# Optimization experiments

Hardware: AMD Instinct MI355X
Metric: run time of the kernel (lower is better)

Reference implementation:

```python
import jax, jax.numpy as jnp
import numpy as np

D = 2048      # d_model
FF = 8192     # d_ff
S = 4096      # seq_len == max_len
EPS = 1.1920929e-07  # torch.finfo(float32).eps (nn.RMSNorm default when eps=None)
SCALE = float(np.sqrt(D))


def _rms_norm(x, w):
    # x: [S, D]
    return x * jax.lax.rsqrt(jnp.mean(x * x, axis=-1, keepdims=True) + EPS) * w


def _rope(x, cos, sin):
    # x: [S, D]; cos/sin: [S, D/2]
    x1, x2 = jnp.split(x, 2, axis=-1)
    return jnp.concatenate([x1 * cos - x2 * sin, x1 * sin + x2 * cos], axis=-1)


def setup_inputs() -> dict:
    key = jax.random.key(0)
    ks = jax.random.split(key, 9)

    def w(k, shape, scale=0.02):
        return jax.random.normal(k, shape, dtype=jnp.float32) * scale

    x = jax.random.normal(ks[0], (S, D), dtype=jnp.float32)
    # torch nn.Linear stores weight as [out, in]; forward is x @ W.T
    wq = w(ks[1], (D, D))
    wk = w(ks[2], (D, D))
    wv = w(ks[3], (D, D))
    wo = w(ks[4], (D, D))
    w_gate = w(ks[5], (FF, D))
    w_up = w(ks[6], (FF, D))
    w_down = w(ks[7], (D, FF))
    w_rn1 = jnp.ones((D,), dtype=jnp.float32)
    w_rn2 = jnp.ones((D,), dtype=jnp.float32)
    # RoPE caches (buffers)
    freqs = 1.0 / 10000.0 ** (jnp.arange(0, D, 2, dtype=jnp.float32) / D)
    t = jnp.arange(S, dtype=jnp.float32)
    angles = jnp.outer(t, freqs)  # [S, D/2]
    cos = jnp.cos(angles)
    sin = jnp.sin(angles)
    return dict(x=x, w_rn1=w_rn1, wq=wq, wk=wk, wv=wv, wo=wo,
                w_rn2=w_rn2, w_gate=w_gate, w_up=w_up, w_down=w_down,
                cos=cos, sin=sin)


def reference(x, w_rn1, wq, wk, wv, wo, w_rn2, w_gate, w_up, w_down, cos, sin):
    h = _rms_norm(x, w_rn1)                      # [S, D]
    q = _rope(h @ wq.T, cos, sin)                # [S, D]
    k = _rope(h @ wk.T, cos, sin)                # [S, D]
    v = h @ wv.T                                 # [S, D]
    attn = jax.nn.softmax(q @ k.T / SCALE, axis=-1)  # [S, S]
    x = x + (attn @ v) @ wo.T                    # residual 1
    h = _rms_norm(x, w_rn2)
    ffn = (jax.nn.silu(h @ w_gate.T) * (h @ w_up.T)) @ w_down.T  # SwiGLU
    return x + ffn
```

## Files before the change

kernel.cpp:

```cpp
#include <hip/hip_runtime.h>

#define S_LEN 4096
#define D_MODEL 2048
#define FF_DIM 8192
#define QKV_LD 6144

typedef __attribute__((ext_vector_type(8))) short s16x8;
typedef __attribute__((ext_vector_type(4))) short s16x4;
typedef __attribute__((ext_vector_type(4))) float f32x4;

__device__ __forceinline__ short f2bf(float f) {
  union { float f; unsigned u; } c; c.f = f;
  unsigned r = (c.u + 0x7fffu + ((c.u >> 16) & 1u)) >> 16;
  return (short)r;
}
__device__ __forceinline__ float bf2f(short s) {
  union { unsigned u; float f; } c; c.u = ((unsigned)(unsigned short)s) << 16;
  return c.f;
}

#define GLDS16(g, l) __builtin_amdgcn_global_load_lds( \
    (const __attribute__((address_space(1))) unsigned*)(g), \
    (__attribute__((address_space(3))) unsigned*)(l), 16, 0, 0)

template <int N> __device__ __forceinline__ void waitvm() {
  if constexpr (N == 0)      asm volatile("s_waitcnt vmcnt(0)" ::: "memory");
  else if constexpr (N == 3) asm volatile("s_waitcnt vmcnt(3)" ::: "memory");
  else if constexpr (N == 4) asm volatile("s_waitcnt vmcnt(4)" ::: "memory");
  else if constexpr (N == 6) asm volatile("s_waitcnt vmcnt(6)" ::: "memory");
  else                       asm volatile("s_waitcnt vmcnt(8)" ::: "memory");
}

__device__ __forceinline__ int swz(int byte_off) {
  return byte_off ^ (((byte_off >> 9) & 1) << 5);
}

__global__ void conv_f32_bf16(const float* __restrict__ in, short* __restrict__ out, long n) {
  long i = ((long)blockIdx.x * blockDim.x + threadIdx.x) * 8;
  if (i >= n) return;
  f32x4 a = *(const f32x4*)(in + i);
  f32x4 b = *(const f32x4*)(in + i + 4);
  s16x8 o;
  o[0] = f2bf(a[0]); o[1] = f2bf(a[1]); o[2] = f2bf(a[2]); o[3] = f2bf(a[3]);
  o[4] = f2bf(b[0]); o[5] = f2bf(b[1]); o[6] = f2bf(b[2]); o[7] = f2bf(b[3]);
  *(s16x8*)(out + i) = o;
}

__global__ void rmsnorm_kernel(const float* __restrict__ x, const float* __restrict__ w,
                               short* __restrict__ out) {
  const int row = blockIdx.x;
  const int t = threadIdx.x;
  const float* xr = x + (long)row * D_MODEL;
  f32x4 v0 = ((const f32x4*)xr)[t];
  f32x4 v1 = ((const f32x4*)xr)[256 + t];
  float ss = v0[0]*v0[0] + v0[1]*v0[1] + v0[2]*v0[2] + v0[3]*v0[3]
           + v1[0]*v1[0] + v1[1]*v1[1] + v1[2]*v1[2] + v1[3]*v1[3];
  #pragma unroll
  for (int o = 32; o > 0; o >>= 1) ss += __shfl_xor(ss, o, 64);
  __shared__ float red[4];
  if ((t & 63) == 0) red[t >> 6] = ss;
  __syncthreads();
  ss = red[0] + red[1] + red[2] + red[3];
  float scale = rsqrtf(ss * (1.0f / D_MODEL) + 1.1920929e-07f);
  f32x4 w0 = ((const f32x4*)w)[t];
  f32x4 w1 = ((const f32x4*)w)[256 + t];
  s16x4 o0, o1;
  #pragma unroll
  for (int i = 0; i < 4; i++) {
    o0[i] = f2bf(v0[i] * scale * w0[i]);
    o1[i] = f2bf(v1[i] * scale * w1[i]);
  }
  short* orow = out + (long)row * D_MODEL;
  ((s16x4*)orow)[t] = o0;
  ((s16x4*)orow)[256 + t] = o1;
}

__global__ void rope_kernel(short* __restrict__ qkv,
                            const float* __restrict__ cosb, const float* __restrict__ sinb) {
  const int s = blockIdx.x;
  short* row = qkv + (long)s * QKV_LD + (blockIdx.y ? D_MODEL : 0);
  const int j = threadIdx.x * 4;
  f32x4 c = *(const f32x4*)(cosb + (long)s * (D_MODEL / 2) + j);
  f32x4 sn = *(const f32x4*)(sinb + (long)s * (D_MODEL / 2) + j);
  s16x4 x1 = *(s16x4*)(row + j);
  s16x4 x2 = *(s16x4*)(row + (D_MODEL / 2) + j);
  s16x4 o1, o2;
  #pragma unroll
  for (int i = 0; i < 4; i++) {
    float a = bf2f(x1[i]), b = bf2f(x2[i]);
    o1[i] = f2bf(a * c[i] - b * sn[i]);
    o2[i] = f2bf(a * sn[i] + b * c[i]);
  }
  *(s16x4*)(row + j) = o1;
  *(s16x4*)(row + (D_MODEL / 2) + j) = o2;
}

__global__ void transpose_kernel(const short* __restrict__ in, short* __restrict__ out,
                                 int R, int C, int ld) {
  __shared__ short tile[32][33];
  const int bx = blockIdx.x * 32, by = blockIdx.y * 32;
  const int x = threadIdx.x, y = threadIdx.y;
  #pragma unroll
  for (int i = 0; i < 32; i += 8) tile[y + i][x] = in[(long)(by + y + i) * ld + bx + x];
  __syncthreads();
  #pragma unroll
  for (int i = 0; i < 32; i += 8) out[(long)(bx + y + i) * R + by + x] = tile[x][y + i];
}

__global__ void softmax_kernel(const float* __restrict__ sraw, short* __restrict__ pb) {
  const int row = blockIdx.x;
  const int t = threadIdx.x;
  const float* rp = sraw + (long)row * S_LEN;
  f32x4 v[4];
  #pragma unroll
  for (int i = 0; i < 4; i++) v[i] = ((const f32x4*)rp)[i * 256 + t];
  float m = -1e30f;
  #pragma unroll
  for (int i = 0; i < 4; i++)
    m = fmaxf(m, fmaxf(fmaxf(v[i][0], v[i][1]), fmaxf(v[i][2], v[i][3])));
  #pragma unroll
  for (int o = 32; o > 0; o >>= 1) m = fmaxf(m, __shfl_xor(m, o, 64));
  __shared__ float redm[4], reds[4];
  if ((t & 63) == 0) redm[t >> 6] = m;
  __syncthreads();
  m = fmaxf(fmaxf(redm[0], redm[1]), fmaxf(redm[2], redm[3]));
  float sum = 0.f;
  #pragma unroll
  for (int i = 0; i < 4; i++) {
    #pragma unroll
    for (int j = 0; j < 4; j++) { v[i][j] = __expf(v[i][j] - m); sum += v[i][j]; }
  }
  #pragma unroll
  for (int o = 32; o > 0; o >>= 1) sum += __shfl_xor(sum, o, 64);
  if ((t & 63) == 0) reds[t >> 6] = sum;
  __syncthreads();
  sum = reds[0] + reds[1] + reds[2] + reds[3];
  float inv = 1.0f / sum;
  short* prow = pb + (long)row * S_LEN;
  #pragma unroll
  for (int i = 0; i < 4; i++) {
    s16x4 o;
    #pragma unroll
    for (int j = 0; j < 4; j++) o[j] = f2bf(v[i][j] * inv);
    ((s16x4*)prow)[i * 256 + t] = o;
  }
}

template <int BN, int EPI>
__global__ __launch_bounds__(512)
void gemm_pipe(const short* __restrict__ A, const short* __restrict__ B,
               float* __restrict__ Cf, short* __restrict__ Cb,
               const short* __restrict__ gmul, const float* __restrict__ res,
               int K, int lda, int ldb, int ldc, float scale) {
  constexpr int BM = 256;
  constexpr int LPS = (BN == 256) ? 4 : 3;
  constexpr int WR = (BN == 256) ? 2 : 4;
  constexpr int WC = 8 / WR;
  constexpr int MF = BM / WR / 16;
  constexpr int NF = BN / WC / 16;
  __shared__ short lds[4][(BM + BN) * 32];

  const int t = threadIdx.x;
  const int lane = t & 63, wid = t >> 6;
  const int wr = wid / WC, wc = wid % WC;
  const int llo = lane & 15, lhi = lane >> 4;

  const int nwg = gridDim.x * gridDim.y;
  int bid = blockIdx.y * gridDim.x + blockIdx.x;
  bid = (bid & 7) * (nwg >> 3) + (bid >> 3);
  const long m0 = (long)(bid / gridDim.x) * BM;
  const long n0 = (long)(bid % gridDim.x) * BN;

  const int ca0 = t, ca1 = t + 512;
  auto src_off = [&](int c, long r0, long ld) {
    int sb = swz(c * 16);
    return (r0 + (sb >> 6)) * ld + ((sb & 63) >> 1);
  };
  const long as0 = src_off(ca0, m0, lda);
  const long as1 = src_off(ca1, m0, lda);
  const long bs0 = src_off(ca0, n0, ldb);
  const long bs1 = (BN == 256) ? src_off(ca1, n0, ldb) : 0;

  f32x4 acc[MF][NF];
  #pragma unroll
  for (int m = 0; m < MF; m++)
    #pragma unroll
    for (int n = 0; n < NF; n++) acc[m][n] = (f32x4)(0.f);

  int aoff[MF], boff[NF];
  #pragma unroll
  for (int m = 0; m < MF; m++) {
    int b = (wr * (BM / WR) + m * 16 + llo) * 64 + lhi * 16;
    aoff[m] = swz(b) >> 1;
  }
  #pragma unroll
  for (int n = 0; n < NF; n++) {
    int b = (wc * (BN / WC) + n * 16 + llo) * 64 + lhi * 16;
    boff[n] = swz(b) >> 1;
  }

  auto stage = [&](int ks) {
    short* la = (short*)lds[ks & 3];
    short* lb = la + BM * 32;
    const long kk = (long)ks * 32;
    GLDS16(A + as0 + kk, la + ca0 * 8);
    GLDS16(A + as1 + kk, la + ca1 * 8);
    GLDS16(B + bs0 + kk, lb + ca0 * 8);
    if constexpr (BN == 256) GLDS16(B + bs1 + kk, lb + ca1 * 8);
  };

  auto phase_compute = [&](int ks) {
    const short* la = (const short*)lds[ks & 3];
    const short* lb = la + BM * 32;
    s16x8 af[MF], bf[NF];
    #pragma unroll
    for (int m = 0; m < MF; m++) af[m] = *(const s16x8*)(la + aoff[m]);
    #pragma unroll
    for (int n = 0; n < NF; n++) bf[n] = *(const s16x8*)(lb + boff[n]);
    __builtin_amdgcn_s_setprio(1);
    #pragma unroll
    for (int m = 0; m < MF; m++)
      #pragma unroll
      for (int n = 0; n < NF; n++)
        acc[m][n] = __builtin_amdgcn_mfma_f32_16x16x32_bf16(af[m], bf[n], acc[m][n], 0, 0, 0);
    __builtin_amdgcn_s_setprio(0);
  };

  const int NPH = K >> 5;
  stage(0); stage(1); stage(2);
  waitvm<2 * LPS>();
  __builtin_amdgcn_s_barrier();
  for (int p = 0; p < NPH - 3; ++p) {
    stage(p + 3);
    phase_compute(p);
    waitvm<2 * LPS>();
    __builtin_amdgcn_s_barrier();
  }
  phase_compute(NPH - 3);
  waitvm<LPS>();
  __builtin_amdgcn_s_barrier();
  phase_compute(NPH - 2);
  waitvm<0>();
  __builtin_amdgcn_s_barrier();
  phase_compute(NPH - 1);

  #pragma unroll
  for (int m = 0; m < MF; m++) {
    const long row0 = m0 + wr * (BM / WR) + m * 16 + lhi * 4;
    #pragma unroll
    for (int n = 0; n < NF; n++) {
      const long col = n0 + wc * (BN / WC) + n * 16 + llo;
      #pragma unroll
      for (int r = 0; r < 4; r++) {
        float v = acc[m][n][r];
        long idx = (row0 + r) * (long)ldc + col;
        if (EPI == 0) {
          Cb[idx] = f2bf(v);
        } else if (EPI == 1) {
          Cb[idx] = f2bf(v / (1.0f + __expf(-v)));
        } else if (EPI == 2) {
          Cb[idx] = f2bf(bf2f(gmul[idx]) * v);
        } else if (EPI == 3) {
          Cf[idx] = v * scale;
        } else {
          Cf[idx] = res[idx] + v;
        }
      }
    }
  }
}

extern "C" void kernel_launch(void* const* d_in, const int* in_sizes, int n_in,
                              void* d_out, int out_size, void* d_ws, size_t ws_size,
                              hipStream_t stream) {
  const float* x      = (const float*)d_in[0];
  const float* w_rn1  = (const float*)d_in[1];
  const float* wq     = (const float*)d_in[2];
  const float* wk     = (const float*)d_in[3];
  const float* wv     = (const float*)d_in[4];
  const float* wo     = (const float*)d_in[5];
  const float* w_rn2  = (const float*)d_in[6];
  const float* w_gate = (const float*)d_in[7];
  const float* w_up   = (const float*)d_in[8];
  const float* w_down = (const float*)d_in[9];
  const float* cosb   = (const float*)d_in[10];
  const float* sinb   = (const float*)d_in[11];
  float* out = (float*)d_out;

  const long S = S_LEN, D = D_MODEL, FF = FF_DIM;
  char* ws = (char*)d_ws;
  size_t off = 0;
  auto alloc = [&](size_t bytes) { void* p = ws + off; off += (bytes + 255) & ~(size_t)255; return p; };

  short* qkv  = (short*)alloc(S * QKV_LD * 2);
  short* vT   = (short*)alloc(D * S * 2);
  short* hb   = (short*)alloc(S * D * 2);
  float* x1   = (float*)alloc(S * D * 4);
  short* wbuf = (short*)alloc(FF * D * 2);
  char*  u2   = (char*)alloc(S * S * 4);
  float* sraw = (float*)u2;
  short* gbuf = (short*)u2;
  short* pb   = (short*)alloc(S * S * 2);

  const float inv_scale = 1.0f / sqrtf((float)D_MODEL);
  const long DD = D * D, FD = FF * D;
  const int convDD = (int)(DD / 8 / 256), convFD = (int)(FD / 8 / 256);
  dim3 blk(256), blk5(512);
  dim3 gQKV(3 * D_MODEL / 256, S_LEN / 256);
  dim3 gS(S_LEN / 256, S_LEN / 256);
  dim3 gN2048(D_MODEL / 128, S_LEN / 256);
  dim3 gF(FF_DIM / 256, S_LEN / 256);

  rmsnorm_kernel<<<S_LEN, 256, 0, stream>>>(x, w_rn1, hb);
  conv_f32_bf16<<<convDD, blk, 0, stream>>>(wq, wbuf, DD);
  conv_f32_bf16<<<convDD, blk, 0, stream>>>(wk, wbuf + DD, DD);
  conv_f32_bf16<<<convDD, blk, 0, stream>>>(wv, wbuf + 2 * DD, DD);
  gemm_pipe<256, 0><<<gQKV, blk5, 0, stream>>>(hb, wbuf, nullptr, qkv, nullptr, nullptr,
                                               D_MODEL, D_MODEL, D_MODEL, QKV_LD, 1.f);
  rope_kernel<<<dim3(S_LEN, 2), blk, 0, stream>>>(qkv, cosb, sinb);
  transpose_kernel<<<dim3(D_MODEL / 32, S_LEN / 32), dim3(32, 8), 0, stream>>>(
      qkv + 2 * D_MODEL, vT, S_LEN, D_MODEL, QKV_LD);
  gemm_pipe<256, 3><<<gS, blk5, 0, stream>>>(qkv, qkv + D_MODEL, sraw, nullptr, nullptr, nullptr,
                                             D_MODEL, QKV_LD, QKV_LD, S_LEN, inv_scale);
  softmax_kernel<<<S_LEN, 256, 0, stream>>>(sraw, pb);
  gemm_pipe<128, 0><<<gN2048, blk5, 0, stream>>>(pb, vT, nullptr, qkv + 2 * D_MODEL, nullptr, nullptr,
                                                 S_LEN, S_LEN, S_LEN, QKV_LD, 1.f);
  conv_f32_bf16<<<convDD, blk, 0, stream>>>(wo, wbuf, DD);
  gemm_pipe<128, 4><<<gN2048, blk5, 0, stream>>>(qkv + 2 * D_MODEL, wbuf, x1, nullptr, nullptr, x,
                                                 D_MODEL, QKV_LD, D_MODEL, D_MODEL, 1.f);
  rmsnorm_kernel<<<S_LEN, 256, 0, stream>>>(x1, w_rn2, hb);
  conv_f32_bf16<<<convFD, blk, 0, stream>>>(w_gate, wbuf, FD);
  gemm_pipe<256, 1><<<gF, blk5, 0, stream>>>(hb, wbuf, nullptr, gbuf, nullptr, nullptr,
                                             D_MODEL, D_MODEL, D_MODEL, FF_DIM, 1.f);
  conv_f32_bf16<<<convFD, blk, 0, stream>>>(w_up, wbuf, FD);
  gemm_pipe<256, 2><<<gF, blk5, 0, stream>>>(hb, wbuf, nullptr, gbuf, gbuf, nullptr,
                                             D_MODEL, D_MODEL, D_MODEL, FF_DIM, 1.f);
  conv_f32_bf16<<<convFD, blk, 0, stream>>>(w_down, wbuf, FD);
  gemm_pipe<128, 4><<<gN2048, blk5, 0, stream>>>(gbuf, wbuf, out, nullptr, nullptr, x1,
                                                 FF_DIM, FF_DIM, FF_DIM, D_MODEL, 1.f);
}
```

Measured before the change: 889.9 us.

## Replace GEMM with 8-phase ping-pong pipelined kernels using 64-wide K tiles

Replaces the generic 4-stage K=32 GEMM with two specialised kernels (256x256 and 256x128 tiles) that use K=64 tiles, a new 8-way XOR LDS swizzle, and a fine-grained schedule. The schedule splits each tile into quadrant MFMA phases, interleaving global-to-LDS loads of parts of the next tile with LDS reads and MFMAs, separated by barriers. The aim is better overlap of memory traffic with matrix-core work and fewer LDS bank conflicts. It adds many barriers and assumes K is a multiple of 128 (n256) or 64 (n128).

```diff
diff --git a/kernel.cpp b/kernel.cpp
--- a/kernel.cpp
+++ b/kernel.cpp
@@ -23,17 +23,13 @@
     (const __attribute__((address_space(1))) unsigned*)(g), \
     (__attribute__((address_space(3))) unsigned*)(l), 16, 0, 0)
 
-template <int N> __device__ __forceinline__ void waitvm() {
-  if constexpr (N == 0)      asm volatile("s_waitcnt vmcnt(0)" ::: "memory");
-  else if constexpr (N == 3) asm volatile("s_waitcnt vmcnt(3)" ::: "memory");
-  else if constexpr (N == 4) asm volatile("s_waitcnt vmcnt(4)" ::: "memory");
-  else if constexpr (N == 6) asm volatile("s_waitcnt vmcnt(6)" ::: "memory");
-  else                       asm volatile("s_waitcnt vmcnt(8)" ::: "memory");
-}
-
-__device__ __forceinline__ int swz(int byte_off) {
-  return byte_off ^ (((byte_off >> 9) & 1) << 5);
-}
+__device__ __forceinline__ int swz(int b) {
+  return b ^ (((b >> 7) & 7) << 4);
+}
+
+#define BAR()   __builtin_amdgcn_s_barrier()
+#define LGKM0() asm volatile("s_waitcnt lgkmcnt(0)" ::: "memory")
+#define VMC(n)  asm volatile("s_waitcnt vmcnt(" #n ")" ::: "memory")
 
 __global__ void conv_f32_bf16(const float* __restrict__ in, short* __restrict__ out, long n) {
   long i = ((long)blockIdx.x * blockDim.x + threadIdx.x) * 8;
@@ -146,128 +142,239 @@
   }
 }
 
-template <int BN, int EPI>
+template <int EPI>
+__device__ __forceinline__ void epi_store(float v, long idx, float* Cf, short* Cb,
+                                          const short* gmul, const float* res, float scale) {
+  if (EPI == 0)      Cb[idx] = f2bf(v);
+  else if (EPI == 1) Cb[idx] = f2bf(v / (1.0f + __expf(-v)));
+  else if (EPI == 2) Cb[idx] = f2bf(bf2f(gmul[idx]) * v);
+  else if (EPI == 3) Cf[idx] = v * scale;
+  else               Cf[idx] = res[idx] + v;
+}
+
+template <int EPI>
 __global__ __launch_bounds__(512)
-void gemm_pipe(const short* __restrict__ A, const short* __restrict__ B,
-               float* __restrict__ Cf, short* __restrict__ Cb,
-               const short* __restrict__ gmul, const float* __restrict__ res,
-               int K, int lda, int ldb, int ldc, float scale) {
-  constexpr int BM = 256;
-  constexpr int LPS = (BN == 256) ? 4 : 3;
-  constexpr int WR = (BN == 256) ? 2 : 4;
-  constexpr int WC = 8 / WR;
-  constexpr int MF = BM / WR / 16;
-  constexpr int NF = BN / WC / 16;
-  __shared__ short lds[4][(BM + BN) * 32];
-
+void gemm8p_n256(const short* __restrict__ A, const short* __restrict__ B,
+                 float* __restrict__ Cf, short* __restrict__ Cb,
+                 const short* __restrict__ gmul, const float* __restrict__ res,
+                 int K, int lda, int ldb, int ldc, float scale) {
+  __shared__ short lds[2][32768];
   const int t = threadIdx.x;
   const int lane = t & 63, wid = t >> 6;
-  const int wr = wid / WC, wc = wid % WC;
+  const int wr = wid >> 2, wc = wid & 3;
   const int llo = lane & 15, lhi = lane >> 4;
 
   const int nwg = gridDim.x * gridDim.y;
   int bid = blockIdx.y * gridDim.x + blockIdx.x;
   bid = (bid & 7) * (nwg >> 3) + (bid >> 3);
-  const long m0 = (long)(bid / gridDim.x) * BM;
-  const long n0 = (long)(bid % gridDim.x) * BN;
-
-  const int ca0 = t, ca1 = t + 512;
-  auto src_off = [&](int c, long r0, long ld) {
-    int sb = swz(c * 16);
-    return (r0 + (sb >> 6)) * ld + ((sb & 63) >> 1);
+  const long m0 = (long)(bid / gridDim.x) * 256;
+  const long n0 = (long)(bid % gridDim.x) * 256;
+
+  const int c0 = t, c1 = t + 512;
+  const int sb0 = swz(c0 * 16), sb1 = swz(c1 * 16);
+  const short* srcA0 = A + (m0 + (sb0 >> 7)) * (long)lda + ((sb0 & 127) >> 1);
+  const short* srcA1 = A + (m0 + (sb1 >> 7)) * (long)lda + ((sb1 & 127) >> 1);
+  const short* srcB0 = B + (n0 + (sb0 >> 7)) * (long)ldb + ((sb0 & 127) >> 1);
+  const short* srcB1 = B + (n0 + (sb1 >> 7)) * (long)ldb + ((sb1 & 127) >> 1);
+  const long dA = 128L * lda, dB = 128L * ldb;
+  const int NT = K >> 6, NI = NT >> 1;
+
+  int aof[4][2], bof[2][2];
+  #pragma unroll
+  for (int mf = 0; mf < 4; mf++)
+    #pragma unroll
+    for (int ks = 0; ks < 2; ks++)
+      aof[mf][ks] = swz((wr * 128 + mf * 16 + llo) * 128 + ks * 64 + lhi * 16) >> 1;
+  #pragma unroll
+  for (int nf = 0; nf < 2; nf++)
+    #pragma unroll
+    for (int ks = 0; ks < 2; ks++)
+      bof[nf][ks] = swz(32768 + (wc * 64 + nf * 16 + llo) * 128 + ks * 64 + lhi * 16) >> 1;
+
+  f32x4 acc[8][4];
+  #pragma unroll
+  for (int m = 0; m < 8; m++)
+    #pragma unroll
+    for (int n = 0; n < 4; n++) acc[m][n] = (f32x4)(0.f);
+
+  s16x8 ar[4][2], b0r[2][2], b1r[2][2];
+
+  auto stage = [&](int tt, int p) {
+    if (tt >= NT) return;
+    short* dst = (short*)lds[tt & 1] + p * 8192;
+    const long kk = (long)tt * 64;
+    const short *s0, *s1;
+    if (p == 0)      { s0 = srcA0;      s1 = srcA1; }
+    else if (p == 1) { s0 = srcA0 + dA; s1 = srcA1 + dA; }
+    else if (p == 2) { s0 = srcB0;      s1 = srcB1; }
+    else             { s0 = srcB0 + dB; s1 = srcB1 + dB; }
+    GLDS16(s0 + kk, dst + c0 * 8);
+    GLDS16(s1 + kk, dst + c1 * 8);
   };
-  const long as0 = src_off(ca0, m0, lda);
-  const long as1 = src_off(ca1, m0, lda);
-  const long bs0 = src_off(ca0, n0, ldb);
-  const long bs1 = (BN == 256) ? src_off(ca1, n0, ldb) : 0;
-
-  f32x4 acc[MF][NF];
-  #pragma unroll
-  for (int m = 0; m < MF; m++)
-    #pragma unroll
-    for (int n = 0; n < NF; n++) acc[m][n] = (f32x4)(0.f);
-
-  int aoff[MF], boff[NF];
-  #pragma unroll
-  for (int m = 0; m < MF; m++) {
-    int b = (wr * (BM / WR) + m * 16 + llo) * 64 + lhi * 16;
-    aoff[m] = swz(b) >> 1;
-  }
-  #pragma unroll
-  for (int n = 0; n < NF; n++) {
-    int b = (wc * (BN / WC) + n * 16 + llo) * 64 + lhi * 16;
-    boff[n] = swz(b) >> 1;
-  }
-
-  auto stage = [&](int ks) {
-    short* la = (short*)lds[ks & 3];
-    short* lb = la + BM * 32;
-    const long kk = (long)ks * 32;
-    GLDS16(A + as0 + kk, la + ca0 * 8);
-    GLDS16(A + as1 + kk, la + ca1 * 8);
-    GLDS16(B + bs0 + kk, lb + ca0 * 8);
-    if constexpr (BN == 256) GLDS16(B + bs1 + kk, lb + ca1 * 8);
+
+#define LDA6(BUF, MH) { const short* lp = (const short*)lds[BUF]; \
+  _Pragma("unroll") for (int mf = 0; mf < 4; mf++) \
+  _Pragma("unroll") for (int ks = 0; ks < 2; ks++) \
+    ar[mf][ks] = *(const s16x8*)(lp + aof[mf][ks] + (MH) * 4096); }
+#define LDB6(BUF, NH, DST) { const short* lp = (const short*)lds[BUF]; \
+  _Pragma("unroll") for (int nf = 0; nf < 2; nf++) \
+  _Pragma("unroll") for (int ks = 0; ks < 2; ks++) \
+    DST[nf][ks] = *(const s16x8*)(lp + bof[nf][ks] + (NH) * 2048); }
+#define MFMAQ6(MH, NH, BR) { __builtin_amdgcn_s_setprio(1); \
+  _Pragma("unroll") for (int ks = 0; ks < 2; ks++) \
+  _Pragma("unroll") for (int mf = 0; mf < 4; mf++) \
+  _Pragma("unroll") for (int nf = 0; nf < 2; nf++) \
+    acc[(MH)*4+mf][(NH)*2+nf] = __builtin_amdgcn_mfma_f32_16x16x32_bf16( \
+        ar[mf][ks], BR[nf][ks], acc[(MH)*4+mf][(NH)*2+nf], 0, 0, 0); \
+  __builtin_amdgcn_s_setprio(0); }
+
+  stage(0, 0); stage(0, 1); stage(0, 2); stage(0, 3);
+  stage(1, 2); stage(1, 3);
+  VMC(4); BAR();
+
+  for (int it = 0; it < NI; ++it) {
+    const int tt = it * 2;
+    const bool last = (it == NI - 1);
+    LDA6(0, 0); LDB6(0, 0, b0r); stage(tt + 1, 0);
+    BAR(); LGKM0(); MFMAQ6(0, 0, b0r); BAR();
+    LDB6(0, 1, b1r); stage(tt + 1, 1);
+    BAR(); LGKM0(); MFMAQ6(0, 1, b1r); BAR();
+    LDA6(0, 1); stage(tt + 2, 2);
+    BAR(); LGKM0(); MFMAQ6(1, 1, b1r); BAR();
+    stage(tt + 2, 3);
+    if (last) { VMC(0); } else { VMC(4); }
+    BAR(); MFMAQ6(1, 0, b0r); BAR();
+    LDA6(1, 0); LDB6(1, 0, b0r); stage(tt + 2, 0);
+    BAR(); LGKM0(); MFMAQ6(0, 0, b0r); BAR();
+    LDB6(1, 1, b1r); stage(tt + 2, 1);
+    BAR(); LGKM0(); MFMAQ6(0, 1, b1r); BAR();
+    LDA6(1, 1); stage(tt + 3, 2);
+    BAR(); LGKM0(); MFMAQ6(1, 1, b1r); BAR();
+    stage(tt + 3, 3);
+    if (last) { VMC(0); } else { VMC(4); }
+    BAR(); MFMAQ6(1, 0, b0r); BAR();
+  }
+
+  #pragma unroll
+  for (int mf = 0; mf < 8; mf++) {
+    const long row0 = m0 + wr * 128 + mf * 16 + lhi * 4;
+    #pragma unroll
+    for (int j = 0; j < 4; j++) {
+      const long col = n0 + wc * 64 + (j >> 1) * 32 + (j & 1) * 16 + llo;
+      #pragma unroll
+      for (int r = 0; r < 4; r++)
+        epi_store<EPI>(acc[mf][j][r], (row0 + r) * (long)ldc + col, Cf, Cb, gmul, res, scale);
+    }
+  }
+#undef LDA6
+#undef LDB6
+#undef MFMAQ6
+}
+
+template <int EPI>
+__global__ __launch_bounds__(512)
+void gemm8p_n128(const short* __restrict__ A, const short* __restrict__ B,
+                 float* __restrict__ Cf, short* __restrict__ Cb,
+                 const short* __restrict__ gmul, const float* __restrict__ res,
+                 int K, int lda, int ldb, int ldc, float scale) {
+  __shared__ short lds[3][24576];
+  const int t = threadIdx.x;
+  const int lane = t & 63, wid = t >> 6;
+  const int wr = wid >> 1, wc = wid & 1;
+  const int llo = lane & 15, lhi = lane >> 4;
+
+  const int nwg = gridDim.x * gridDim.y;
+  int bid = blockIdx.y * gridDim.x + blockIdx.x;
+  bid = (bid & 7) * (nwg >> 3) + (bid >> 3);
+  const long m0 = (long)(bid / gridDim.x) * 256;
+  const long n0 = (long)(bid % gridDim.x) * 128;
+
+  const int c0 = t, c1 = t + 512;
+  const int sb0 = swz(c0 * 16), sb1 = swz(c1 * 16);
+  const short* srcA0 = A + (m0 + (sb0 >> 7)) * (long)lda + ((sb0 & 127) >> 1);
+  const short* srcA1 = A + (m0 + (sb1 >> 7)) * (long)lda + ((sb1 & 127) >> 1);
+  const short* srcB0 = B + (n0 + (sb0 >> 7)) * (long)ldb + ((sb0 & 127) >> 1);
+  const short* srcB1 = B + (n0 + (sb1 >> 7)) * (long)ldb + ((sb1 & 127) >> 1);
+  const long dA = 128L * lda;
+  const int NT = K >> 6;
+
+  int aof[4][2], bof[2][2];
+  #pragma unroll
+  for (int mf = 0; mf < 4; mf++)
+    #pragma unroll
+    for (int ks = 0; ks < 2; ks++)
+      aof[mf][ks] = swz((wr * 64 + mf * 16 + llo) * 128 + ks * 64 + lhi * 16) >> 1;
+  #pragma unroll
+  for (int nf = 0; nf < 2; nf++)
+    #pragma unroll
+    for (int ks = 0; ks < 2; ks++)
+      bof[nf][ks] = swz(32768 + (wc * 64 + nf * 16 + llo) * 128 + ks * 64 + lhi * 16) >> 1;
+
+  f32x4 acc[4][4];
+  #pragma unroll
+  for (int m = 0; m < 4; m++)
+    #pragma unroll
+    for (int n = 0; n < 4; n++) acc[m][n] = (f32x4)(0.f);
+
+  s16x8 ar[4][2], br[2][2];
+
+  auto stage = [&](int tt, int slot, int p) {
+    if (tt >= NT) return;
+    short* dst = (short*)lds[slot] + p * 8192;
+    const long kk = (long)tt * 64;
+    const short *s0, *s1;
+    if (p == 0)      { s0 = srcA0;      s1 = srcA1; }
+    else if (p == 1) { s0 = srcA0 + dA; s1 = srcA1 + dA; }
+    else             { s0 = srcB0;      s1 = srcB1; }
+    GLDS16(s0 + kk, dst + c0 * 8);
+    GLDS16(s1 + kk, dst + c1 * 8);
   };
 
-  auto phase_compute = [&](int ks) {
-    const short* la = (const short*)lds[ks & 3];
-    const short* lb = la + BM * 32;
-    s16x8 af[MF], bf[NF];
-    #pragma unroll
-    for (int m = 0; m < MF; m++) af[m] = *(const s16x8*)(la + aoff[m]);
-    #pragma unroll
-    for (int n = 0; n < NF; n++) bf[n] = *(const s16x8*)(lb + boff[n]);
-    __builtin_amdgcn_s_setprio(1);
-    #pragma unroll
-    for (int m = 0; m < MF; m++)
+#define LDA3(CUR) { const short* lp = (const short*)lds[CUR]; \
+  _Pragma("unroll") for (int mf = 0; mf < 4; mf++) \
+  _Pragma("unroll") for (int ks = 0; ks < 2; ks++) \
+    ar[mf][ks] = *(const s16x8*)(lp + aof[mf][ks]); }
+#define LDB3(CUR, NH) { const short* lp = (const short*)lds[CUR]; \
+  _Pragma("unroll") for (int nf = 0; nf < 2; nf++) \
+  _Pragma("unroll") for (int ks = 0; ks < 2; ks++) \
+    br[nf][ks] = *(const s16x8*)(lp + bof[nf][ks] + (NH) * 2048); }
+#define MFMAQ3(NH) { __builtin_amdgcn_s_setprio(1); \
+  _Pragma("unroll") for (int ks = 0; ks < 2; ks++) \
+  _Pragma("unroll") for (int mf = 0; mf < 4; mf++) \
+  _Pragma("unroll") for (int nf = 0; nf < 2; nf++) \
+    acc[mf][(NH)*2+nf] = __builtin_amdgcn_mfma_f32_16x16x32_bf16( \
+        ar[mf][ks], br[nf][ks], acc[mf][(NH)*2+nf], 0, 0, 0); \
+  __builtin_amdgcn_s_setprio(0); }
+
+  stage(0, 0, 0); stage(0, 0, 1); stage(0, 0, 2);
+  stage(1, 1, 0); stage(1, 1, 1); stage(1, 1, 2);
+  VMC(6); BAR();
+
+  int cur = 0;
+  for (int tt = 0; tt < NT; ++tt) {
+    const int s2 = (cur >= 1) ? cur - 1 : 2;
+    LDA3(cur); LDB3(cur, 0); stage(tt + 2, s2, 0); stage(tt + 2, s2, 1);
+    BAR(); LGKM0(); MFMAQ3(0); BAR();
+    LDB3(cur, 1); stage(tt + 2, s2, 2);
+    if (tt >= NT - 2) { VMC(0); } else { VMC(6); }
+    BAR(); LGKM0(); MFMAQ3(1); BAR();
+    cur = (cur == 2) ? 0 : cur + 1;
+  }
+
+  #pragma unroll
+  for (int mf = 0; mf < 4; mf++) {
+    const long row0 = m0 + wr * 64 + mf * 16 + lhi * 4;
+    #pragma unroll
+    for (int j = 0; j < 4; j++) {
+      const long col = n0 + wc * 64 + (j >> 1) * 32 + (j & 1) * 16 + llo;
       #pragma unroll
-      for (int n = 0; n < NF; n++)
-        acc[m][n] = __builtin_amdgcn_mfma_f32_16x16x32_bf16(af[m], bf[n], acc[m][n], 0, 0, 0);
-    __builtin_amdgcn_s_setprio(0);
-  };
-
-  const int NPH = K >> 5;
-  stage(0); stage(1); stage(2);
-  waitvm<2 * LPS>();
-  __builtin_amdgcn_s_barrier();
-  for (int p = 0; p < NPH - 3; ++p) {
-    stage(p + 3);
-    phase_compute(p);
-    waitvm<2 * LPS>();
-    __builtin_amdgcn_s_barrier();
-  }
-  phase_compute(NPH - 3);
-  waitvm<LPS>();
-  __builtin_amdgcn_s_barrier();
-  phase_compute(NPH - 2);
-  waitvm<0>();
-  __builtin_amdgcn_s_barrier();
-  phase_compute(NPH - 1);
-
-  #pragma unroll
-  for (int m = 0; m < MF; m++) {
-    const long row0 = m0 + wr * (BM / WR) + m * 16 + lhi * 4;
-    #pragma unroll
-    for (int n = 0; n < NF; n++) {
-      const long col = n0 + wc * (BN / WC) + n * 16 + llo;
-      #pragma unroll
-      for (int r = 0; r < 4; r++) {
-        float v = acc[m][n][r];
-        long idx = (row0 + r) * (long)ldc + col;
-        if (EPI == 0) {
-          Cb[idx] = f2bf(v);
-        } else if (EPI == 1) {
-          Cb[idx] = f2bf(v / (1.0f + __expf(-v)));
-        } else if (EPI == 2) {
-          Cb[idx] = f2bf(bf2f(gmul[idx]) * v);
-        } else if (EPI == 3) {
-          Cf[idx] = v * scale;
-        } else {
-          Cf[idx] = res[idx] + v;
-        }
-      }
+      for (int r = 0; r < 4; r++)
+        epi_store<EPI>(acc[mf][j][r], (row0 + r) * (long)ldc + col, Cf, Cb, gmul, res, scale);
     }
   }
+#undef LDA3
+#undef LDB3
+#undef MFMAQ3
 }
 
 extern "C" void kernel_launch(void* const* d_in, const int* in_sizes, int n_in,
@@ -315,27 +422,27 @@
   conv_f32_bf16<<<convDD, blk, 0, stream>>>(wq, wbuf, DD);
   conv_f32_bf16<<<convDD, blk, 0, stream>>>(wk, wbuf + DD, DD);
   conv_f32_bf16<<<convDD, blk, 0, stream>>>(wv, wbuf + 2 * DD, DD);
-  gemm_pipe<256, 0><<<gQKV, blk5, 0, stream>>>(hb, wbuf, nullptr, qkv, nullptr, nullptr,
-                                               D_MODEL, D_MODEL, D_MODEL, QKV_LD, 1.f);
+  gemm8p_n256<0><<<gQKV, blk5, 0, stream>>>(hb, wbuf, nullptr, qkv, nullptr, nullptr,
+                                            D_MODEL, D_MODEL, D_MODEL, QKV_LD, 1.f);
   rope_kernel<<<dim3(S_LEN, 2), blk, 0, stream>>>(qkv, cosb, sinb);
   transpose_kernel<<<dim3(D_MODEL / 32, S_LEN / 32), dim3(32, 8), 0, stream>>>(
       qkv + 2 * D_MODEL, vT, S_LEN, D_MODEL, QKV_LD);
-  gemm_pipe<256, 3><<<gS, blk5, 0, stream>>>(qkv, qkv + D_MODEL, sraw, nullptr, nullptr, nullptr,
-                                             D_MODEL, QKV_LD, QKV_LD, S_LEN, inv_scale);
+  gemm8p_n256<3><<<gS, blk5, 0, stream>>>(qkv, qkv + D_MODEL, sraw, nullptr, nullptr, nullptr,
+                                          D_MODEL, QKV_LD, QKV_LD, S_LEN, inv_scale);
   softmax_kernel<<<S_LEN, 256, 0, stream>>>(sraw, pb);
-  gemm_pipe<128, 0><<<gN2048, blk5, 0, stream>>>(pb, vT, nullptr, qkv + 2 * D_MODEL, nullptr, nullptr,
-                                                 S_LEN, S_LEN, S_LEN, QKV_LD, 1.f);
+  gemm8p_n128<0><<<gN2048, blk5, 0, stream>>>(pb, vT, nullptr, qkv + 2 * D_MODEL, nullptr, nullptr,
+                                              S_LEN, S_LEN, S_LEN, QKV_LD, 1.f);
   conv_f32_bf16<<<convDD, blk, 0, stream>>>(wo, wbuf, DD);
-  gemm_pipe<128, 4><<<gN2048, blk5, 0, stream>>>(qkv + 2 * D_MODEL, wbuf, x1, nullptr, nullptr, x,
-                                                 D_MODEL, QKV_LD, D_MODEL, D_MODEL, 1.f);
+  gemm8p_n128<4><<<gN2048, blk5, 0, stream>>>(qkv + 2 * D_MODEL, wbuf, x1, nullptr, nullptr, x,
+                                              D_MODEL, QKV_LD, D_MODEL, D_MODEL, 1.f);
   rmsnorm_kernel<<<S_LEN, 256, 0, stream>>>(x1, w_rn2, hb);
   conv_f32_bf16<<<convFD, blk, 0, stream>>>(w_gate, wbuf, FD);
-  gemm_pipe<256, 1><<<gF, blk5, 0, stream>>>(hb, wbuf, nullptr, gbuf, nullptr, nullptr,
-                                             D_MODEL, D_MODEL, D_MODEL, FF_DIM, 1.f);
+  gemm8p_n256<1><<<gF, blk5, 0, stream>>>(hb, wbuf, nullptr, gbuf, nullptr, nullptr,
+                                          D_MODEL, D_MODEL, D_MODEL, FF_DIM, 1.f);
   conv_f32_bf16<<<convFD, blk, 0, stream>>>(w_up, wbuf, FD);
-  gemm_pipe<256, 2><<<gF, blk5, 0, stream>>>(hb, wbuf, nullptr, gbuf, gbuf, nullptr,
-                                             D_MODEL, D_MODEL, D_MODEL, FF_DIM, 1.f);
+  gemm8p_n256<2><<<gF, blk5, 0, stream>>>(hb, wbuf, nullptr, gbuf, gbuf, nullptr,
+                                          D_MODEL, D_MODEL, D_MODEL, FF_DIM, 1.f);
   conv_f32_bf16<<<convFD, blk, 0, stream>>>(w_down, wbuf, FD);
-  gemm_pipe<128, 4><<<gN2048, blk5, 0, stream>>>(gbuf, wbuf, out, nullptr, nullptr, x1,
-                                                 FF_DIM, FF_DIM, FF_DIM, D_MODEL, 1.f);
-}
+  gemm8p_n128<4><<<gN2048, blk5, 0, stream>>>(gbuf, wbuf, out, nullptr, nullptr, x1,
+                                              FF_DIM, FF_DIM, FF_DIM, D_MODEL, 1.f);
+}
```

After: 858.9 us. -3.5%, faster.
